# Performance work log

Measured on AMD Instinct MI355X. Metric: run time of the kernel, lower is better.

Reference implementation:

```python
import jax, jax.numpy as jnp
import numpy as np
from math import factorial, sqrt

MUL = 64            # common multiplicity of all irreps
BASE = 9            # base_dim for 0e+1o+2e = 1+3+5
LS = [0, 1, 2]      # l of each base irrep
OFFS = [0, 1, 4]    # offset of each base irrep inside base_dim
INSTR = [(0,0,0),(0,1,1),(0,2,2),(1,0,1),(1,1,0),(1,1,2),(1,2,1),(2,0,2),(2,1,1),(2,2,0),(2,2,2)]
Z = 50000           # number of edges (batch)


def _w3j_complex(l1, l2, l3):
    # Racah formula for the (complex-basis) Wigner 3j symbol.
    f = factorial
    W = np.zeros((2*l1+1, 2*l2+1, 2*l3+1))
    delta = sqrt(f(l1+l2-l3)*f(l1-l2+l3)*f(-l1+l2+l3)/f(l1+l2+l3+1))
    for m1 in range(-l1, l1+1):
        for m2 in range(-l2, l2+1):
            m3 = -m1 - m2
            if abs(m3) > l3:
                continue
            pre = (-1)**(l1-l2-m3) * delta * sqrt(
                f(l1+m1)*f(l1-m1)*f(l2+m2)*f(l2-m2)*f(l3+m3)*f(l3-m3))
            s = 0.0
            for t in range(0, l1+l2-l3+1):
                dens = [t, l3-l2+t+m1, l3-l1+t-m2, l1+l2-l3-t, l1-t-m1, l2-t+m2]
                if any(d < 0 for d in dens):
                    continue
                s += (-1)**t / np.prod([float(f(d)) for d in dens])
            W[m1+l1, m2+l2, m3+l3] = pre * s
    return W


def _c2r(l):
    # complex->real spherical harmonic change of basis
    U = np.zeros((2*l+1, 2*l+1), dtype=complex)
    U[l, l] = 1.0
    s2 = 1.0/sqrt(2.0)
    for m in range(1, l+1):
        U[l+m, l+m] = (-1)**m * s2
        U[l+m, l-m] = s2
        U[l-m, l-m] = 1j * s2
        U[l-m, l+m] = -1j * (-1)**m * s2
    return U


def _w3j_real(l1, l2, l3):
    C = _w3j_complex(l1, l2, l3).astype(complex)
    R = np.einsum('ax,by,cz,xyz->abc', _c2r(l1), _c2r(l2), _c2r(l3), C)
    # real if l1+l2+l3 even, purely imaginary otherwise
    return R.real if np.abs(R.real).max() >= np.abs(R.imag).max() else R.imag


def _build_w3j():
    # dense buffer of shape (num_paths, k_out, i_in1, j_in2) with CG blocks
    P = len(INSTR)
    W = np.zeros((P, BASE, BASE, BASE), dtype=np.float32)
    counts = {}
    for ins in INSTR:
        counts[ins[2]] = counts.get(ins[2], 0) + 1
    for p, (i1, i2, io) in enumerate(INSTR):
        l1, l2, lo = LS[i1], LS[i2], LS[io]
        blk = _w3j_real(l1, l2, lo)  # (2l1+1, 2l2+1, 2lo+1)
        # 'component' normalization, 'uuu' mode: alpha = sqrt((2*lo+1)/n_paths_to_out)
        alpha = sqrt((2*lo+1) / counts[io])
        o1, o2, oo = OFFS[i1], OFFS[i2], OFFS[io]
        W[p, oo:oo+2*lo+1, o1:o1+2*l1+1, o2:o2+2*l2+1] = alpha * blk.transpose(2, 0, 1)
    return jnp.asarray(W)


def setup_inputs() -> dict:
    key = jax.random.key(0)
    k1, k2, k3 = jax.random.split(key, 3)
    x1 = jax.random.normal(k1, (Z, MUL*BASE), dtype=jnp.float32)
    x2 = jax.random.normal(k2, (Z, MUL*BASE), dtype=jnp.float32)
    # 'uniform' init -> unit-variance uniform on [-sqrt(3), sqrt(3)], shape (mul, num_paths)
    weights = jax.random.uniform(k3, (MUL, len(INSTR)), dtype=jnp.float32,
                                 minval=-sqrt(3.0), maxval=sqrt(3.0))
    return {"x1": x1, "x2": x2, "weights": weights, "w3j": _build_w3j()}


def reference(x1, x2, weights, w3j):
    x1 = x1.reshape(-1, MUL, BASE)   # (z, u, i)
    x2 = x2.reshape(-1, MUL, BASE)   # (z, u, j)
    # 'up,pkij->ukij' : fold per-channel per-path weights into the CG tensor
    ww3j = jnp.einsum('up,pkij->ukij', weights, w3j)
    # 'zui,zuj,ukij->zuk' : channel-wise bilinear CG contraction
    return jnp.einsum('zui,zuj,ukij->zuk', x1, x2, ww3j)
```

## Files before the change

### kernel.cpp

```cpp
#include <hip/hip_runtime.h>


#define MUL   64
#define BASE  9
#define NPATH 11
#define ZT    64

__global__ __launch_bounds__(256) void fold_kernel(
    const float* __restrict__ weights,
    const float* __restrict__ w3j,
    float*       __restrict__ ww)
{
    int u = blockIdx.x / 3;
    int t = (blockIdx.x % 3) * 256 + threadIdx.x;
    if (t >= 729) return;
    float acc = 0.f;
#pragma unroll
    for (int p = 0; p < NPATH; ++p)
        acc = fmaf(weights[u * NPATH + p], w3j[p * 729 + t], acc);
    ww[u * 729 + t] = acc;
}

__global__ __launch_bounds__(256) void tp_kernel(
    const float* __restrict__ x1,
    const float* __restrict__ x2,
    const float* __restrict__ ww,
    float*       __restrict__ out,
    int Z, int n_zt)
{
    int b    = blockIdx.x;
    int xcd  = b & 7;
    int j    = b >> 3;
    int uc   = j & 15;
    int q    = j >> 4;
    int zt   = xcd + 8 * q;
    if (zt >= n_zt) return;

    int wave = threadIdx.x >> 6;
    int lane = threadIdx.x & 63;
    int u    = __builtin_amdgcn_readfirstlane(uc * 4 + wave);
    int z    = zt * ZT + lane;
    bool active = (z < Z);

    const float* __restrict__ wrow = ww + u * 729;

    const float* p1 = x1 + (size_t)z * 576 + u * 9;
    const float* p2 = x2 + (size_t)z * 576 + u * 9;

    float X1[BASE], X2[BASE];
#pragma unroll
    for (int i = 0; i < BASE; ++i) {
        X1[i] = active ? p1[i] : 0.f;
        X2[i] = active ? p2[i] : 0.f;
    }

    float r[BASE * BASE];
#pragma unroll
    for (int i = 0; i < BASE; ++i)
#pragma unroll
        for (int jj = 0; jj < BASE; ++jj)
            r[i * BASE + jj] = X1[i] * X2[jj];

    float o[BASE];
#pragma unroll
    for (int k = 0; k < BASE; ++k) o[k] = 0.f;
#pragma unroll
    for (int t = 0; t < BASE * BASE; ++t)
#pragma unroll
        for (int k = 0; k < BASE; ++k)
            o[k] = fmaf(wrow[k * 81 + t], r[t], o[k]);

    float* po = out + (size_t)z * 576 + u * 9;
    if (active) {
#pragma unroll
        for (int k = 0; k < BASE; ++k) po[k] = o[k];
    }
}

extern "C" void kernel_launch(void* const* d_in, const int* in_sizes, int n_in,
                              void* d_out, int out_size, void* d_ws, size_t ws_size,
                              hipStream_t stream) {
    const float* x1  = (const float*)d_in[0];
    const float* x2  = (const float*)d_in[1];
    const float* w   = (const float*)d_in[2];
    const float* w3j = (const float*)d_in[3];
    float* out = (float*)d_out;
    float* ww  = (float*)d_ws;

    int Z = in_sizes[0] / (MUL * BASE);

    fold_kernel<<<MUL * 3, 256, 0, stream>>>(w, w3j, ww);

    int n_zt = (Z + ZT - 1) / ZT;
    int Q    = (n_zt + 7) / 8;
    int grid = 8 * 16 * Q;
    tp_kernel<<<grid, 256, 0, stream>>>(x1, x2, ww, out, Z, n_zt);
}
```

Before: 317.3 us.

## Stage inputs/outputs through LDS with float4 coalescing and sparse CG path loops

```diff
diff --git a/kernel.cpp b/kernel.cpp
--- a/kernel.cpp
+++ b/kernel.cpp
@@ -1,10 +1,14 @@
 #include <hip/hip_runtime.h>
 
 
-#define MUL   64
-#define BASE  9
-#define NPATH 11
-#define ZT    64
+#define MUL    64
+#define BASE   9
+#define NPATH  11
+#define ZT     64
+#define UC     4
+#define NCH    4
+#define URANGE (UC*NCH)
+#define PAD    38
 
 __global__ __launch_bounds__(256) void fold_kernel(
     const float* __restrict__ weights,
@@ -21,6 +25,42 @@
     ww[u * 729 + t] = acc;
 }
 
+__device__ __forceinline__ void stage_in(
+    const float* __restrict__ x1, const float* __restrict__ x2,
+    float* s1, float* s2, int z0, int ucbase, int Z, int t)
+{
+    for (int e = t; e < ZT * 9; e += 256) {
+        int z  = e / 9;
+        int c4 = (e - z * 9) * 4;
+        if (z0 + z < Z) {
+            int g = (z0 + z) * (MUL * BASE) + ucbase * BASE + c4;
+            float4 v1 = *(const float4*)(x1 + g);
+            float4 v2 = *(const float4*)(x2 + g);
+            int a = z * PAD + c4;
+            *(float2*)(s1 + a)     = make_float2(v1.x, v1.y);
+            *(float2*)(s1 + a + 2) = make_float2(v1.z, v1.w);
+            *(float2*)(s2 + a)     = make_float2(v2.x, v2.y);
+            *(float2*)(s2 + a + 2) = make_float2(v2.z, v2.w);
+        }
+    }
+}
+
+__device__ __forceinline__ void stage_out(
+    float* __restrict__ out, const float* so, int z0, int ucbase, int Z, int t)
+{
+    for (int e = t; e < ZT * 9; e += 256) {
+        int z  = e / 9;
+        int c4 = (e - z * 9) * 4;
+        if (z0 + z < Z) {
+            int a = z * PAD + c4;
+            float2 lo = *(const float2*)(so + a);
+            float2 hi = *(const float2*)(so + a + 2);
+            int g = (z0 + z) * (MUL * BASE) + ucbase * BASE + c4;
+            *(float4*)(out + g) = make_float4(lo.x, lo.y, hi.x, hi.y);
+        }
+    }
+}
+
 __global__ __launch_bounds__(256) void tp_kernel(
     const float* __restrict__ x1,
     const float* __restrict__ x2,
@@ -28,53 +68,77 @@
     float*       __restrict__ out,
     int Z, int n_zt)
 {
-    int b    = blockIdx.x;
-    int xcd  = b & 7;
-    int j    = b >> 3;
-    int uc   = j & 15;
-    int q    = j >> 4;
-    int zt   = xcd + 8 * q;
+    __shared__ float s1[ZT * PAD];
+    __shared__ float s2[ZT * PAD];
+    __shared__ float so[ZT * PAD];
+
+    int g    = blockIdx.x;
+    int xcd  = g & 7;
+    int loc  = g >> 3;
+    int ur   = loc & 3;
+    int zt   = (loc >> 2) * 8 + xcd;
     if (zt >= n_zt) return;
 
-    int wave = threadIdx.x >> 6;
-    int lane = threadIdx.x & 63;
-    int u    = __builtin_amdgcn_readfirstlane(uc * 4 + wave);
-    int z    = zt * ZT + lane;
-    bool active = (z < Z);
+    int t    = threadIdx.x;
+    int wave = t >> 6;
+    int lane = t & 63;
+    int z0   = zt * ZT;
+    int u0   = ur * URANGE;
 
-    const float* __restrict__ wrow = ww + u * 729;
+    constexpr int P1[NPATH] = {0,0,0,1,1,1,1,2,2,2,2};
+    constexpr int P2[NPATH] = {0,1,2,0,1,1,2,0,1,2,2};
+    constexpr int PO[NPATH] = {0,1,2,1,0,2,1,2,1,0,2};
+    constexpr int NL[3]  = {1,3,5};
+    constexpr int OFF[3] = {0,1,4};
 
-    const float* p1 = x1 + (size_t)z * 576 + u * 9;
-    const float* p2 = x2 + (size_t)z * 576 + u * 9;
+#pragma unroll 1
+    for (int c = 0; c < NCH; ++c) {
+        __syncthreads();
+        stage_in(x1, x2, s1, s2, z0, u0 + c * UC, Z, t);
+        if (c > 0) stage_out(out, so, z0, u0 + (c - 1) * UC, Z, t);
+        __syncthreads();
 
-    float X1[BASE], X2[BASE];
+        int u = u0 + c * UC + wave;
+        u = __builtin_amdgcn_readfirstlane(u);
+        const float* __restrict__ wrow = ww + u * 729;
+
+        float X1[BASE], X2[BASE];
+        int base = lane * PAD + wave * BASE;
 #pragma unroll
-    for (int i = 0; i < BASE; ++i) {
-        X1[i] = active ? p1[i] : 0.f;
-        X2[i] = active ? p2[i] : 0.f;
-    }
+        for (int i = 0; i < BASE; ++i) {
+            X1[i] = s1[base + i];
+            X2[i] = s2[base + i];
+        }
 
-    float r[BASE * BASE];
+        float o[BASE];
 #pragma unroll
-    for (int i = 0; i < BASE; ++i)
+        for (int k = 0; k < BASE; ++k) o[k] = 0.f;
+
 #pragma unroll
-        for (int jj = 0; jj < BASE; ++jj)
-            r[i * BASE + jj] = X1[i] * X2[jj];
+        for (int p = 0; p < NPATH; ++p) {
+            const int o1 = OFF[P1[p]], n1 = NL[P1[p]];
+            const int o2 = OFF[P2[p]], n2 = NL[P2[p]];
+            const int oo = OFF[PO[p]], no = NL[PO[p]];
+#pragma unroll
+            for (int i = 0; i < n1; ++i) {
+                float a = X1[o1 + i];
+#pragma unroll
+                for (int j = 0; j < n2; ++j) {
+                    float rv = a * X2[o2 + j];
+#pragma unroll
+                    for (int k = 0; k < no; ++k)
+                        o[oo + k] = fmaf(wrow[(oo + k) * 81 + (o1 + i) * 9 + (o2 + j)],
+                                         rv, o[oo + k]);
+                }
+            }
+        }
 
-    float o[BASE];
-#pragma unroll
-    for (int k = 0; k < BASE; ++k) o[k] = 0.f;
-#pragma unroll
-    for (int t = 0; t < BASE * BASE; ++t)
 #pragma unroll
         for (int k = 0; k < BASE; ++k)
-            o[k] = fmaf(wrow[k * 81 + t], r[t], o[k]);
-
-    float* po = out + (size_t)z * 576 + u * 9;
-    if (active) {
-#pragma unroll
-        for (int k = 0; k < BASE; ++k) po[k] = o[k];
+            so[base + k] = o[k];
     }
+    __syncthreads();
+    stage_out(out, so, z0, u0 + (NCH - 1) * UC, Z, t);
 }
 
 extern "C" void kernel_launch(void* const* d_in, const int* in_sizes, int n_in,
@@ -92,7 +156,7 @@
     fold_kernel<<<MUL * 3, 256, 0, stream>>>(w, w3j, ww);
 
     int n_zt = (Z + ZT - 1) / ZT;
-    int Q    = (n_zt + 7) / 8;
-    int grid = 8 * 16 * Q;
+    int q    = (n_zt + 7) / 8;
+    int grid = 8 * 4 * q;
     tp_kernel<<<grid, 256, 0, stream>>>(x1, x2, ww, out, Z, n_zt);
 }
```

After: 360.2 us. 1.13x slower.

## Pack sparse CG paths and process four channels per thread with float4 I/O

Applied to the files above, without the earlier changes.

```diff
diff --git a/kernel.cpp b/kernel.cpp
--- a/kernel.cpp
+++ b/kernel.cpp
@@ -4,76 +4,110 @@
 #define MUL   64
 #define BASE  9
 #define NPATH 11
-#define ZT    64
+#define NC    363
+#define CPAD  368
 
-__global__ __launch_bounds__(256) void fold_kernel(
+#define PATH_TABLES \
+    constexpr int P1[NPATH] = {0,0,0,1,1,1,1,2,2,2,2}; \
+    constexpr int P2[NPATH] = {0,1,2,0,1,1,2,0,1,2,2}; \
+    constexpr int PO[NPATH] = {0,1,2,1,0,2,1,2,1,0,2}; \
+    constexpr int NL[3]  = {1,3,5}; \
+    constexpr int OFF[3] = {0,1,4};
+
+__global__ __launch_bounds__(384) void fold_pack_kernel(
     const float* __restrict__ weights,
     const float* __restrict__ w3j,
-    float*       __restrict__ ww)
+    float*       __restrict__ cw)
 {
-    int u = blockIdx.x / 3;
-    int t = (blockIdx.x % 3) * 256 + threadIdx.x;
-    if (t >= 729) return;
-    float acc = 0.f;
-#pragma unroll
-    for (int p = 0; p < NPATH; ++p)
-        acc = fmaf(weights[u * NPATH + p], w3j[p * 729 + t], acc);
-    ww[u * 729 + t] = acc;
+    PATH_TABLES
+    constexpr int SZ[NPATH] = {1,9,25,9,9,45,45,25,45,25,125};
+
+    int u   = blockIdx.x;
+    int idx = threadIdx.x;
+    if (idx >= NC) return;
+
+    int p = 0, rem = idx;
+    while (rem >= SZ[p]) { rem -= SZ[p]; ++p; }
+    int n2 = NL[P2[p]], no = NL[PO[p]];
+    int i  = rem / (n2 * no);
+    int r  = rem - i * (n2 * no);
+    int j  = r / no;
+    int k  = r - j * no;
+    int gi = OFF[P1[p]] + i;
+    int gj = OFF[P2[p]] + j;
+    int gk = OFF[PO[p]] + k;
+
+    cw[u * CPAD + idx] = weights[u * NPATH + p] * w3j[p * 729 + gk * 81 + gi * 9 + gj];
 }
 
-__global__ __launch_bounds__(256) void tp_kernel(
+__global__ __launch_bounds__(256, 3) void tp_kernel(
     const float* __restrict__ x1,
     const float* __restrict__ x2,
-    const float* __restrict__ ww,
+    const float* __restrict__ cw,
     float*       __restrict__ out,
-    int Z, int n_zt)
+    int Z)
 {
-    int b    = blockIdx.x;
-    int xcd  = b & 7;
-    int j    = b >> 3;
-    int uc   = j & 15;
-    int q    = j >> 4;
-    int zt   = xcd + 8 * q;
-    if (zt >= n_zt) return;
+    PATH_TABLES
 
+    int g    = blockIdx.x;
+    int zt   = g >> 2;
+    int grp  = g & 3;
     int wave = threadIdx.x >> 6;
     int lane = threadIdx.x & 63;
-    int u    = __builtin_amdgcn_readfirstlane(uc * 4 + wave);
-    int z    = zt * ZT + lane;
-    bool active = (z < Z);
 
-    const float* __restrict__ wrow = ww + u * 729;
+    int z    = zt * 64 + lane;
+    bool act = (z < Z);
+    int zc   = act ? z : (Z - 1);
 
-    const float* p1 = x1 + (size_t)z * 576 + u * 9;
-    const float* p2 = x2 + (size_t)z * 576 + u * 9;
+    int u0 = __builtin_amdgcn_readfirstlane((grp * 4 + wave) * 4);
 
-    float X1[BASE], X2[BASE];
+    const float4* a4 = (const float4*)(x1 + (size_t)zc * (MUL * BASE) + u0 * BASE);
+    const float4* b4 = (const float4*)(x2 + (size_t)zc * (MUL * BASE) + u0 * BASE);
+
+    float4 Av[9], Bv[9];
 #pragma unroll
-    for (int i = 0; i < BASE; ++i) {
-        X1[i] = active ? p1[i] : 0.f;
-        X2[i] = active ? p2[i] : 0.f;
+    for (int i = 0; i < 9; ++i) { Av[i] = a4[i]; Bv[i] = b4[i]; }
+    const float* X1 = (const float*)Av;
+    const float* X2 = (const float*)Bv;
+
+    float4 Ov[9];
+    float* O = (float*)Ov;
+#pragma unroll
+    for (int k = 0; k < 36; ++k) O[k] = 0.f;
+
+#pragma unroll
+    for (int uu = 0; uu < 4; ++uu) {
+        const float* __restrict__ cr = cw + (size_t)(u0 + uu) * CPAD;
+        const float* xa = X1 + uu * BASE;
+        const float* xb = X2 + uu * BASE;
+        float*       oo = O  + uu * BASE;
+
+        int c = 0;
+#pragma unroll
+        for (int p = 0; p < NPATH; ++p) {
+            const int o1 = OFF[P1[p]], n1 = NL[P1[p]];
+            const int o2 = OFF[P2[p]], n2 = NL[P2[p]];
+            const int og = OFF[PO[p]], no = NL[PO[p]];
+#pragma unroll
+            for (int i = 0; i < n1; ++i) {
+                float a = xa[o1 + i];
+#pragma unroll
+                for (int j = 0; j < n2; ++j) {
+                    float rv = a * xb[o2 + j];
+#pragma unroll
+                    for (int k = 0; k < no; ++k) {
+                        oo[og + k] = fmaf(cr[c], rv, oo[og + k]);
+                        ++c;
+                    }
+                }
+            }
+        }
     }
 
-    float r[BASE * BASE];
+    if (act) {
+        float4* o4 = (float4*)(out + (size_t)z * (MUL * BASE) + u0 * BASE);
 #pragma unroll
-    for (int i = 0; i < BASE; ++i)
-#pragma unroll
-        for (int jj = 0; jj < BASE; ++jj)
-            r[i * BASE + jj] = X1[i] * X2[jj];
-
-    float o[BASE];
-#pragma unroll
-    for (int k = 0; k < BASE; ++k) o[k] = 0.f;
-#pragma unroll
-    for (int t = 0; t < BASE * BASE; ++t)
-#pragma unroll
-        for (int k = 0; k < BASE; ++k)
-            o[k] = fmaf(wrow[k * 81 + t], r[t], o[k]);
-
-    float* po = out + (size_t)z * 576 + u * 9;
-    if (active) {
-#pragma unroll
-        for (int k = 0; k < BASE; ++k) po[k] = o[k];
+        for (int i = 0; i < 9; ++i) o4[i] = Ov[i];
     }
 }
 
@@ -85,14 +119,13 @@
     const float* w   = (const float*)d_in[2];
     const float* w3j = (const float*)d_in[3];
     float* out = (float*)d_out;
-    float* ww  = (float*)d_ws;
+    float* cw  = (float*)d_ws;
 
     int Z = in_sizes[0] / (MUL * BASE);
 
-    fold_kernel<<<MUL * 3, 256, 0, stream>>>(w, w3j, ww);
+    fold_pack_kernel<<<MUL, 384, 0, stream>>>(w, w3j, cw);
 
-    int n_zt = (Z + ZT - 1) / ZT;
-    int Q    = (n_zt + 7) / 8;
-    int grid = 8 * 16 * Q;
-    tp_kernel<<<grid, 256, 0, stream>>>(x1, x2, ww, out, Z, n_zt);
+    int nzt  = (Z + 63) / 64;
+    int grid = nzt * 4;
+    tp_kernel<<<grid, 256, 0, stream>>>(x1, x2, cw, out, Z);
 }
```

Result: slower. 465.4 us (+46.7%).
